# Optimization experiments

Hardware: AMD Instinct MI355X
Metric: run time of the kernel (lower is better)

Reference implementation:

```python
import jax, jax.numpy as jnp
import numpy as np

K = 128      # scratch_keys_dim
NP = 3       # n_pointers
P = 200      # program_dim
STEPS = 3    # max_program_steps


def _positional_encoding(max_len=50, d=K):
    pos = np.arange(max_len, dtype=np.float32)[:, None]
    div = np.exp(np.arange(0, d, 2, dtype=np.float32) * (-np.log(10000.0) / d))
    pe = np.zeros((max_len, d), dtype=np.float32)
    pe[:, 0::2] = np.sin(pos * div)
    pe[:, 1::2] = np.cos(pos * div)
    return jnp.asarray(pe)


def setup_inputs() -> dict:
    B, I, L, Vin, Vout = 256, 16, 50, 1000, 512
    H = K * NP
    key = jax.random.key(0)
    ks = jax.random.split(key, 8)
    s = 0.05
    return {
        'instructions': jax.random.randint(ks[0], (I, B), 0, Vin),
        'true_actions': jax.random.randint(ks[1], (L, B), 0, Vout),
        'gate_emb': jax.random.normal(ks[2], (Vin, 2), jnp.float32) * s,
        'program_emb': jax.random.normal(ks[3], (Vin, P), jnp.float32) * s,
        'primitive_emb': jax.random.normal(ks[4], (Vin, Vout), jnp.float32) * s,
        'w_ih': jax.random.normal(ks[5], (3 * H, P), jnp.float32) * s,
        'w_hh': jax.random.normal(ks[6], (3 * H, H), jnp.float32) * s,
        'b_ih': jnp.zeros((3 * H,), jnp.float32),
        'b_hh': jnp.zeros((3 * H,), jnp.float32),
        'scratch_keys': _positional_encoding(),
        'init_value': jnp.zeros((Vout,), jnp.float32).at[0].set(1.0),  # one-hot eos
    }


def _gru_cell(x, h, w_ih, w_hh, b_ih, b_hh):
    # torch.nn.GRUCell math
    gi = x @ w_ih.T + b_ih
    gh = h @ w_hh.T + b_hh
    i_r, i_z, i_n = jnp.split(gi, 3, axis=-1)
    h_r, h_z, h_n = jnp.split(gh, 3, axis=-1)
    r = jax.nn.sigmoid(i_r + h_r)
    z = jax.nn.sigmoid(i_z + h_z)
    n = jnp.tanh(i_n + r * h_n)
    return (1.0 - z) * n + z * h


def reference(instructions, true_actions, gate_emb, program_emb, primitive_emb,
              w_ih, w_hh, b_ih, b_hh, scratch_keys, init_value):
    I, B = instructions.shape
    L = true_actions.shape[0]
    keys = scratch_keys[:L]                                    # [L,K], broadcast over batch
    h0 = jnp.tile(scratch_keys[0], (B, NP))                    # [B,3K] init executor hidden
    v0 = jnp.broadcast_to(init_value, (B, L, init_value.shape[0]))  # [B,L,Vout]

    def outer(carry, word):
        h, vals = carry
        gate = jax.nn.softmax(gate_emb[word], axis=-1)         # [B,2] (softmax gate activation)
        program = program_emb[word]                            # [B,P]
        primitive = primitive_emb[word]                        # [B,Vout]
        for _ in range(STEPS):
            read_ptr = h[:, K:2 * K]                           # [B,K]
            write_ptr = h[:, 2 * K:3 * K]                      # [B,K]
            read_attn = jax.nn.softmax(jnp.einsum('bk,lk->bl', read_ptr, keys), axis=-1)
            read_value = jnp.einsum('bl,blv->bv', read_attn, vals)
            # gate-weighted mix of primitive and read value
            new_value = gate[:, :1] * primitive + gate[:, 1:] * read_value   # [B,Vout]
            write_mask = jax.nn.softmax(jnp.einsum('bk,lk->bl', write_ptr, keys), axis=-1)
            vals = write_mask[:, :, None] * new_value[:, None, :] + (1.0 - write_mask[:, :, None]) * vals
            h = _gru_cell(program, h, w_ih, w_hh, b_ih, b_hh)
        return (h, vals), None

    (h, vals), _ = jax.lax.scan(outer, (h0, v0), instructions)
    actions = jnp.transpose(jax.nn.log_softmax(vals, axis=-1), (0, 2, 1))  # [B,Vout,L]
    return actions, true_actions.T
```

## Files before the change

kernel.cpp:

```cpp
#include <hip/hip_runtime.h>
#include <math.h>

#define KK     128
#define HH     384
#define H3     1152
#define PP     200
#define LL     50
#define VV     512
#define BB     256
#define II     16
#define NSTEPS 3

#define NT     1024
#define GRUT   768
#define VP2    258
#define KQP    33

#define GH4G   12
#define GIG    13
#define WQ4H_UI (GH4G * 3 * 384 * 4)
#define WQI_UI  (GIG  * 3 * 384 * 4)

__device__ __forceinline__ int dot4(unsigned a, unsigned b, int c) {
    return __builtin_amdgcn_sdot4((int)a, (int)b, c, false);
}
__device__ __forceinline__ int dot8(unsigned a, unsigned b, int c) {
    return __builtin_amdgcn_sdot8((int)a, (int)b, c, false);
}
__device__ __forceinline__ float rcpf(float x) { return __builtin_amdgcn_rcpf(x); }
__device__ __forceinline__ float sigm(float x) { return rcpf(1.f + __expf(-x)); }
__device__ __forceinline__ float tanh_fast(float x) {
    float xc = fminf(fmaxf(x, -15.f), 15.f);
    float t = __expf(2.f * xc);
    return 1.f - 2.f * rcpf(t + 1.f);
}
__device__ __forceinline__ int q8(float x, float sc) {
    int q = (int)rintf(x * sc);
    return q < -127 ? -127 : (q > 127 ? 127 : q);
}
__device__ __forceinline__ int q4(float x, float sc) {
    int q = (int)rintf(x * sc);
    return q < -7 ? -7 : (q > 7 ? 7 : q);
}

__global__ void wmax_reduce(const float* __restrict__ w_hh,
                            const float* __restrict__ w_ih,
                            const float* __restrict__ prog_emb,
                            unsigned* __restrict__ scales)
{
    int idx = blockIdx.x * 256 + threadIdx.x;
    int stride = gridDim.x * 256;
    float mh = 0.f, mi = 0.f, mp = 0.f;
    for (int i = idx; i < HH * H3; i += stride) mh = fmaxf(mh, fabsf(w_hh[i]));
    for (int i = idx; i < PP * H3; i += stride) mi = fmaxf(mi, fabsf(w_ih[i]));
    for (int i = idx; i < 1000 * PP; i += stride) mp = fmaxf(mp, fabsf(prog_emb[i]));
    #pragma unroll
    for (int mm = 32; mm >= 1; mm >>= 1) {
        mh = fmaxf(mh, __shfl_xor(mh, mm, 64));
        mi = fmaxf(mi, __shfl_xor(mi, mm, 64));
        mp = fmaxf(mp, __shfl_xor(mp, mm, 64));
    }
    if ((threadIdx.x & 63) == 0) {
        atomicMax(scales,     __float_as_uint(mh));
        atomicMax(scales + 1, __float_as_uint(mi));
        atomicMax(scales + 2, __float_as_uint(mp));
    }
}

__global__ void pack_weights(const float* __restrict__ w_hh,
                             const float* __restrict__ w_ih,
                             const unsigned* __restrict__ scales,
                             unsigned* __restrict__ wq)
{
    int idx = blockIdx.x * 256 + threadIdx.x;
    if (idx < WQ4H_UI) {
        const float sc = 7.f * rcpf(fmaxf(__uint_as_float(scales[0]), 1e-20f));
        int u4 = idx >> 2, m = idx & 3;
        int g = u4 / (3 * 384);
        int r = u4 - g * (3 * 384);
        int s = r / 384, t = r - s * 384;
        int j = t + 384 * s, k = 32 * g + 8 * m;
        const float* wr = w_hh + (long)j * HH + k;
        unsigned pw = 0;
        #pragma unroll
        for (int e = 0; e < 8; ++e) pw |= ((unsigned)(q4(wr[e], sc) & 0xF)) << (4 * e);
        wq[idx] = pw;
    } else if (idx < WQ4H_UI + WQI_UI) {
        const float sc = 127.f * rcpf(fmaxf(__uint_as_float(scales[1]), 1e-20f));
        int q = idx - WQ4H_UI;
        int u4 = q >> 2, m = q & 3;
        int g = u4 / (3 * 384);
        int r = u4 - g * (3 * 384);
        int s = r / 384, t = r - s * 384;
        int j = t + 384 * s, k = 16 * g + 4 * m;
        unsigned pw = 0;
        #pragma unroll
        for (int e = 0; e < 4; ++e) {
            float w = (k + e < PP) ? w_ih[(long)j * PP + k + e] : 0.f;
            pw |= ((unsigned)(q8(w, sc) & 255)) << (8 * e);
        }
        wq[WQ4H_UI + u4 * 4 + m] = pw;
    }
}

struct __align__(16) Smem {
    float2 vals[LL * VP2];
    unsigned keysq[LL * KQP + 16] __attribute__((aligned(16)));
    unsigned hq4[2][48]     __attribute__((aligned(16)));
    unsigned hq8[2][96]     __attribute__((aligned(16)));
    unsigned progq[56]      __attribute__((aligned(16)));
    float  raw[4][52], wmw[4][52];
    float  rowoff[52];
    float  partial[4 * 52];
};

__global__ __launch_bounds__(NT)
void symop_main(const int* __restrict__ instr,
                const float* __restrict__ gate_emb,
                const float* __restrict__ program_emb,
                const float* __restrict__ primitive_emb,
                const uint4* __restrict__ wqhh,
                const uint4* __restrict__ wqih,
                const unsigned* __restrict__ scales,
                const float* __restrict__ b_ih,
                const float* __restrict__ b_hh,
                const float* __restrict__ keys_g,
                const float* __restrict__ init_value,
                float* __restrict__ out)
{
    __shared__ Smem sm;

    const int tid  = threadIdx.x;
    const int lane = tid & 63;
    const int wid  = tid >> 6;
    const int b    = blockIdx.x;
    const int gl   = tid >> 1;
    const int koff = tid & 1;

    const float maxH = fmaxf(__uint_as_float(scales[0]), 1e-20f);
    const float maxI = fmaxf(__uint_as_float(scales[1]), 1e-20f);
    const float maxP = fmaxf(__uint_as_float(scales[2]), 1e-20f);
    const float ghs = maxH * (1.f / 49.f);
    const float gis = maxI * maxP * (1.f / 16129.f);
    const float psc = 127.f * rcpf(maxP);
    const float lsc = 1.f / 16129.f;

    float hcur = 0.f;
    if (tid < GRUT) hcur = keys_g[gl & 127];
    for (int idx = tid; idx < LL * 32; idx += NT) {
        int l = idx >> 5, kk = idx & 31;
        const float* kr = keys_g + l * KK + 4 * kk;
        unsigned pw = 0;
        #pragma unroll
        for (int e = 0; e < 4; ++e) pw |= ((unsigned)(q8(kr[e], 127.f) & 255)) << (8 * e);
        sm.keysq[l * KQP + kk] = pw;
    }
    if (tid < 96) {
        unsigned pw = 0;
        #pragma unroll
        for (int e = 0; e < 4; ++e) {
            int q = q8(keys_g[(4 * tid + e) & 127], 127.f);
            pw |= ((unsigned)(q & 255)) << (8 * e);
        }
        sm.hq8[0][tid] = pw;
    } else if (tid >= 128 && tid < 128 + 48) {
        int u = tid - 128;
        unsigned pw = 0;
        #pragma unroll
        for (int e = 0; e < 8; ++e) {
            int q = q4(keys_g[(8 * u + e) & 127], 7.f);
            pw |= ((unsigned)(q & 0xF)) << (4 * e);
        }
        sm.hq4[0][u] = pw;
    }
    for (int idx = tid; idx < LL * 256; idx += NT) {
        int l = idx >> 8, c = idx & 255;
        sm.vals[l * VP2 + c] = *(const float2*)(init_value + 2 * c);
    }
    if (tid >= GRUT && tid < GRUT + 52) {
        int qt = tid - GRUT;
        int w0 = instr[b];
        const float* pg = program_emb + (long)w0 * PP;
        unsigned pw = 0;
        #pragma unroll
        for (int e = 0; e < 4; ++e) {
            int k = 4 * qt + e;
            float v = (k < PP) ? pg[k] : 0.f;
            pw |= ((unsigned)(q8(v, psc) & 255)) << (8 * e);
        }
        sm.progq[qt] = pw;
    }
    __syncthreads();

    float bh0 = 0, bh1 = 0, bh2 = 0, bi0 = 0, bi1 = 0, bi2 = 0;
    if (tid < GRUT) {
        bh0 = b_hh[gl]; bh1 = b_hh[gl + HH]; bh2 = b_hh[gl + 2 * HH];
        bi0 = b_ih[gl]; bi1 = b_ih[gl + HH]; bi2 = b_ih[gl + 2 * HH];
    }
    float gic0 = 0, gic1 = 0, gic2 = 0;
    int   gn0 = 0, gn1 = 0, gn2 = 0;

    if (tid < GRUT) {
        int ia0 = 0, ia1 = 0, ia2 = 0;
        const uint4* wi = wqih + gl;
        const int gs = koff ? 7 : 0, ge = koff ? GIG : 7;
        for (int g = gs; g < ge; ++g) {
            uint4 w0 = wi[(g * 3 + 0) * 384];
            uint4 w1 = wi[(g * 3 + 1) * 384];
            uint4 w2 = wi[(g * 3 + 2) * 384];
            uint4 hp = *(const uint4*)(sm.progq + 4 * g);
            ia0 = dot4(w0.x, hp.x, ia0); ia0 = dot4(w0.y, hp.y, ia0);
            ia0 = dot4(w0.z, hp.z, ia0); ia0 = dot4(w0.w, hp.w, ia0);
            ia1 = dot4(w1.x, hp.x, ia1); ia1 = dot4(w1.y, hp.y, ia1);
            ia1 = dot4(w1.z, hp.z, ia1); ia1 = dot4(w1.w, hp.w, ia1);
            ia2 = dot4(w2.x, hp.x, ia2); ia2 = dot4(w2.y, hp.y, ia2);
            ia2 = dot4(w2.z, hp.z, ia2); ia2 = dot4(w2.w, hp.w, ia2);
        }
        ia0 += __shfl_xor(ia0, 1, 64);
        ia1 += __shfl_xor(ia1, 1, 64);
        ia2 += __shfl_xor(ia2, 1, 64);
        gic0 = bi0 + (float)ia0 * gis;
        gic1 = bi1 + (float)ia1 * gis;
        gic2 = bi2 + (float)ia2 * gis;
    }

    int par = 0;
    for (int i = 0; i < II; ++i) {
        const int word = instr[i * BB + b];
        for (int t = 0; t < NSTEPS; ++t) {
            if (tid < GRUT) {
                int ia0 = 0, ia1 = 0, ia2 = 0;
                const uint4* wp = wqhh + gl;
                const int gb = koff * 6;
                #pragma unroll 2
                for (int gg = 0; gg < 6; ++gg) {
                    const int g = gb + gg;
                    uint4 w0 = wp[(g * 3 + 0) * 384];
                    uint4 w1 = wp[(g * 3 + 1) * 384];
                    uint4 w2 = wp[(g * 3 + 2) * 384];
                    uint4 hp = *(const uint4*)(sm.hq4[par] + 4 * g);
                    ia0 = dot8(w0.x, hp.x, ia0); ia0 = dot8(w0.y, hp.y, ia0);
                    ia0 = dot8(w0.z, hp.z, ia0); ia0 = dot8(w0.w, hp.w, ia0);
                    ia1 = dot8(w1.x, hp.x, ia1); ia1 = dot8(w1.y, hp.y, ia1);
                    ia1 = dot8(w1.z, hp.z, ia1); ia1 = dot8(w1.w, hp.w, ia1);
                    ia2 = dot8(w2.x, hp.x, ia2); ia2 = dot8(w2.y, hp.y, ia2);
                    ia2 = dot8(w2.z, hp.z, ia2); ia2 = dot8(w2.w, hp.w, ia2);
                }
                ia0 += __shfl_xor(ia0, 1, 64);
                ia1 += __shfl_xor(ia1, 1, 64);
                ia2 += __shfl_xor(ia2, 1, 64);
                const float gh0 = bh0 + (float)ia0 * ghs;
                const float gh1 = bh1 + (float)ia1 * ghs;
                const float gh2 = bh2 + (float)ia2 * ghs;

                if (i + 1 < II) {
                    const uint4* wi = wqih + gl;
                    if (t == 1) {
                        gn0 = 0; gn1 = 0; gn2 = 0;
                        if (!koff) {
                            #pragma unroll 2
                            for (int g = 0; g < 7; ++g) {
                                uint4 w0 = wi[(g * 3 + 0) * 384];
                                uint4 w1 = wi[(g * 3 + 1) * 384];
                                uint4 w2 = wi[(g * 3 + 2) * 384];
                                uint4 hp = *(const uint4*)(sm.progq + 4 * g);
                                gn0 = dot4(w0.x, hp.x, gn0); gn0 = dot4(w0.y, hp.y, gn0);
                                gn0 = dot4(w0.z, hp.z, gn0); gn0 = dot4(w0.w, hp.w, gn0);
                                gn1 = dot4(w1.x, hp.x, gn1); gn1 = dot4(w1.y, hp.y, gn1);
                                gn1 = dot4(w1.z, hp.z, gn1); gn1 = dot4(w1.w, hp.w, gn1);
                                gn2 = dot4(w2.x, hp.x, gn2); gn2 = dot4(w2.y, hp.y, gn2);
                                gn2 = dot4(w2.z, hp.z, gn2); gn2 = dot4(w2.w, hp.w, gn2);
                            }
                        }
                    } else if (t == 2) {
                        if (koff) {
                            #pragma unroll 2
                            for (int g = 7; g < GIG; ++g) {
                                uint4 w0 = wi[(g * 3 + 0) * 384];
                                uint4 w1 = wi[(g * 3 + 1) * 384];
                                uint4 w2 = wi[(g * 3 + 2) * 384];
                                uint4 hp = *(const uint4*)(sm.progq + 4 * g);
                                gn0 = dot4(w0.x, hp.x, gn0); gn0 = dot4(w0.y, hp.y, gn0);
                                gn0 = dot4(w0.z, hp.z, gn0); gn0 = dot4(w0.w, hp.w, gn0);
                                gn1 = dot4(w1.x, hp.x, gn1); gn1 = dot4(w1.y, hp.y, gn1);
                                gn1 = dot4(w1.z, hp.z, gn1); gn1 = dot4(w1.w, hp.w, gn1);
                                gn2 = dot4(w2.x, hp.x, gn2); gn2 = dot4(w2.y, hp.y, gn2);
                                gn2 = dot4(w2.z, hp.z, gn2); gn2 = dot4(w2.w, hp.w, gn2);
                            }
                        }
                        const int f0 = gn0 + __shfl_xor(gn0, 1, 64);
                        const int f1 = gn1 + __shfl_xor(gn1, 1, 64);
                        const int f2 = gn2 + __shfl_xor(gn2, 1, 64);
                        gic0 = bi0 + (float)f0 * gis;
                        gic1 = bi1 + (float)f1 * gis;
                        gic2 = bi2 + (float)f2 * gis;
                    }
                }

                const float r = sigm(gic0 + gh0);
                const float z = sigm(gic1 + gh1);
                const float n = tanh_fast(gic2 + r * gh2);
                const float hn = (1.f - z) * n + z * hcur;
                hcur = hn;
                int q8v = ((int)rintf(hn * 127.f)) & 255;
                unsigned v1 = (unsigned)q8v | ((unsigned)(__shfl_down(q8v, 2, 64) & 255) << 8);
                unsigned v2 = v1 | ((unsigned)__shfl_down((int)v1, 4, 64) << 16);
                if (!(tid & 7)) sm.hq8[par ^ 1][tid >> 3] = v2;
                int q4v = ((int)rintf(hn * 7.f)) & 0xF;
                unsigned u1 = (unsigned)q4v | ((unsigned)(__shfl_down(q4v, 2, 64) & 0xF) << 4);
                unsigned u2 = u1 | ((unsigned)(__shfl_down((int)u1, 4, 64) & 0xFF) << 8);
                unsigned u4 = u2 | ((unsigned)__shfl_down((int)u2, 8, 64) << 16);
                if (!(tid & 15)) sm.hq4[par ^ 1][tid >> 4] = u4;
            } else {
                const int w4 = wid - 12;
                float rlog = -1e30f, wlog = -1e30f;
                if (lane < LL) {
                    int ir = 0, iw = 0;
                    const unsigned* kq = sm.keysq + lane * KQP;
                    const uint4* h8r = (const uint4*)(sm.hq8[par] + 32);
                    const uint4* h8w = (const uint4*)(sm.hq8[par] + 64);
                    #pragma unroll
                    for (int o = 0; o < 8; ++o) {
                        uint4 hr = h8r[o], hw = h8w[o];
                        unsigned k0 = kq[4 * o], k1 = kq[4 * o + 1];
                        unsigned k2 = kq[4 * o + 2], k3 = kq[4 * o + 3];
                        ir = dot4(k0, hr.x, ir); ir = dot4(k1, hr.y, ir);
                        ir = dot4(k2, hr.z, ir); ir = dot4(k3, hr.w, ir);
                        iw = dot4(k0, hw.x, iw); iw = dot4(k1, hw.y, iw);
                        iw = dot4(k2, hw.z, iw); iw = dot4(k3, hw.w, iw);
                    }
                    rlog = (float)ir * lsc;
                    wlog = (float)iw * lsc;
                }
                float mr = rlog, mw = wlog;
                #pragma unroll
                for (int mm = 32; mm >= 1; mm >>= 1) {
                    mr = fmaxf(mr, __shfl_xor(mr, mm, 64));
                    mw = fmaxf(mw, __shfl_xor(mw, mm, 64));
                }
                float er = (lane < LL) ? __expf(rlog - mr) : 0.f;
                float ew = (lane < LL) ? __expf(wlog - mw) : 0.f;
                float sr = er, sw = ew;
                #pragma unroll
                for (int mm = 32; mm >= 1; mm >>= 1) {
                    sr += __shfl_xor(sr, mm, 64);
                    sw += __shfl_xor(sw, mm, 64);
                }
                if (lane < LL) {
                    sm.raw[w4][lane] = er * rcpf(sr);
                    sm.wmw[w4][lane] = ew * rcpf(sw);
                }
                const float ge0 = gate_emb[2 * word], ge1 = gate_emb[2 * word + 1];
                const float gmx = fmaxf(ge0, ge1);
                const float e0 = __expf(ge0 - gmx), e1 = __expf(ge1 - gmx);
                const float g0 = e0 * rcpf(e0 + e1), g1 = 1.0f - g0;
                const float* prim = primitive_emb + (long)word * VV;

                const int c = tid - GRUT;
                float2 pr = *(const float2*)(prim + 2 * c);
                float rv0 = 0.f, rv1 = 0.f;
                #pragma unroll 10
                for (int l = 0; l < LL; ++l) {
                    float2 vv = sm.vals[l * VP2 + c];
                    rv0 = fmaf(sm.raw[w4][l], vv.x, rv0);
                    rv1 = fmaf(sm.raw[w4][l], vv.y, rv1);
                }
                const float nv0 = g0 * pr.x + g1 * rv0;
                const float nv1 = g0 * pr.y + g1 * rv1;
                #pragma unroll 10
                for (int l = 0; l < LL; ++l) {
                    float2 vv = sm.vals[l * VP2 + c];
                    const float w = sm.wmw[w4][l];
                    vv.x = fmaf(w, nv0 - vv.x, vv.x);
                    vv.y = fmaf(w, nv1 - vv.y, vv.y);
                    sm.vals[l * VP2 + c] = vv;
                }
                if (t == 0 && i + 1 < II && tid < GRUT + 52) {
                    int qt = tid - GRUT;
                    int wn = instr[(i + 1) * BB + b];
                    const float* pg = program_emb + (long)wn * PP;
                    unsigned pw = 0;
                    #pragma unroll
                    for (int e = 0; e < 4; ++e) {
                        int k = 4 * qt + e;
                        float v = (k < PP) ? pg[k] : 0.f;
                        pw |= ((unsigned)(q8(v, psc) & 255)) << (8 * e);
                    }
                    sm.progq[qt] = pw;
                }
            }
            __syncthreads();
            par ^= 1;
        }
    }

    if (tid < 256) {
        #pragma unroll 5
        for (int l = 0; l < LL; ++l) {
            float2 vv = sm.vals[l * VP2 + tid];
            float e = __expf(vv.x) + __expf(vv.y);
            #pragma unroll
            for (int mm = 32; mm >= 1; mm >>= 1) e += __shfl_xor(e, mm, 64);
            if (lane == 0) sm.partial[wid * 52 + l] = e;
        }
    }
    __syncthreads();
    if (tid < LL) {
        float s = 0.f;
        #pragma unroll
        for (int w = 0; w < 4; ++w) s += sm.partial[w * 52 + tid];
        sm.rowoff[tid] = logf(s);
    }
    __syncthreads();

    if (tid < 256) {
        float* ob0 = out + (long)b * VV * LL + (long)(2 * tid) * LL;
        float* ob1 = ob0 + LL;
        #pragma unroll 5
        for (int l = 0; l < LL; l += 2) {
            float2 va = sm.vals[l * VP2 + tid];
            float2 vb = sm.vals[(l + 1) * VP2 + tid];
            float o0 = sm.rowoff[l], o1 = sm.rowoff[l + 1];
            *(float2*)(ob0 + l) = make_float2(va.x - o0, vb.x - o1);
            *(float2*)(ob1 + l) = make_float2(va.y - o0, vb.y - o1);
        }
    }
}

__global__ void ta_copy(const int* __restrict__ ta, float* __restrict__ out2)
{
    int idx = blockIdx.x * 256 + threadIdx.x;
    if (idx < BB * LL) {
        int b2 = idx / LL, l = idx % LL;
        out2[idx] = (float)ta[l * BB + b2];
    }
}

extern "C" void kernel_launch(void* const* d_in, const int* in_sizes, int n_in,
                              void* d_out, int out_size, void* d_ws, size_t ws_size,
                              hipStream_t stream)
{
    const int*   instr        = (const int*)  d_in[0];
    const int*   true_actions = (const int*)  d_in[1];
    const float* gate_emb     = (const float*)d_in[2];
    const float* program_emb  = (const float*)d_in[3];
    const float* primitive_emb= (const float*)d_in[4];
    const float* w_ih         = (const float*)d_in[5];
    const float* w_hh         = (const float*)d_in[6];
    const float* b_ih         = (const float*)d_in[7];
    const float* b_hh         = (const float*)d_in[8];
    const float* scratch_keys = (const float*)d_in[9];
    const float* init_value   = (const float*)d_in[10];

    unsigned* scales = (unsigned*)d_ws;
    unsigned* wq     = (unsigned*)d_ws + 4;
    const uint4* wqhh = (const uint4*)wq;
    const uint4* wqih = (const uint4*)(wq + WQ4H_UI);

    hipMemsetAsync(scales, 0, 12, stream);
    wmax_reduce<<<256, 256, 0, stream>>>(w_hh, w_ih, program_emb, scales);
    {
        int total = WQ4H_UI + WQI_UI;
        pack_weights<<<(total + 255) / 256, 256, 0, stream>>>(w_hh, w_ih, scales, wq);
    }

    float* out = (float*)d_out;
    float* out_actions = out;
    float* out_ta      = out + (long)BB * VV * LL;

    symop_main<<<BB, NT, 0, stream>>>(instr, gate_emb, program_emb, primitive_emb,
                                      wqhh, wqih, scales, b_ih, b_hh,
                                      scratch_keys, init_value, out_actions);

    ta_copy<<<(BB * LL + 255) / 256, 256, 0, stream>>>(true_actions, out_ta);
}
```

Baseline: 343.3 us.

## Interleave packed GRU weights per thread and compute next input gates in one step

Packed int4 hidden-weight and int8 input-weight tiles are re-laid out so each thread indexes weights by tid with stride 768. Adjacent lanes, which hold the two K-halves of the same row, now read contiguous uint4s, giving better-coalesced global loads. The next instruction's input-gate projection is now computed entirely at step 1 by both K-halves, not split across steps 1 and 2, and its result is held in separate registers until step 2. Both halves now do balanced work, at the cost of padding the input weights with zeros and adding an extra barrier after the prologue.

```diff
diff --git a/kernel.cpp b/kernel.cpp
--- a/kernel.cpp
+++ b/kernel.cpp
@@ -16,10 +16,9 @@
 #define VP2    258
 #define KQP    33
 
-#define GH4G   12
 #define GIG    13
-#define WQ4H_UI (GH4G * 3 * 384 * 4)
-#define WQI_UI  (GIG  * 3 * 384 * 4)
+#define WQ4H_UI (6 * 3 * 768 * 4)
+#define WQI_UI  (7 * 3 * 768 * 4)
 
 __device__ __forceinline__ int dot4(unsigned a, unsigned b, int c) {
     return __builtin_amdgcn_sdot4((int)a, (int)b, c, false);
@@ -76,10 +75,12 @@
     if (idx < WQ4H_UI) {
         const float sc = 7.f * rcpf(fmaxf(__uint_as_float(scales[0]), 1e-20f));
         int u4 = idx >> 2, m = idx & 3;
-        int g = u4 / (3 * 384);
-        int r = u4 - g * (3 * 384);
-        int s = r / 384, t = r - s * 384;
-        int j = t + 384 * s, k = 32 * g + 8 * m;
+        int gg = u4 / (3 * 768);
+        int r  = u4 - gg * (3 * 768);
+        int s  = r / 768, tt = r - s * 768;
+        int gl = tt >> 1, ko = tt & 1;
+        int j = gl + 384 * s;
+        int k = (ko * 6 + gg) * 32 + 8 * m;
         const float* wr = w_hh + (long)j * HH + k;
         unsigned pw = 0;
         #pragma unroll
@@ -89,15 +90,20 @@
         const float sc = 127.f * rcpf(fmaxf(__uint_as_float(scales[1]), 1e-20f));
         int q = idx - WQ4H_UI;
         int u4 = q >> 2, m = q & 3;
-        int g = u4 / (3 * 384);
-        int r = u4 - g * (3 * 384);
-        int s = r / 384, t = r - s * 384;
-        int j = t + 384 * s, k = 16 * g + 4 * m;
-        unsigned pw = 0;
-        #pragma unroll
-        for (int e = 0; e < 4; ++e) {
-            float w = (k + e < PP) ? w_ih[(long)j * PP + k + e] : 0.f;
-            pw |= ((unsigned)(q8(w, sc) & 255)) << (8 * e);
+        int gg = u4 / (3 * 768);
+        int r  = u4 - gg * (3 * 768);
+        int s  = r / 768, tt = r - s * 768;
+        int gl = tt >> 1, ko = tt & 1;
+        int g = ko ? 7 + gg : gg;
+        int j = gl + 384 * s;
+        unsigned pw = 0;
+        if (g < GIG) {
+            int k = 16 * g + 4 * m;
+            #pragma unroll
+            for (int e = 0; e < 4; ++e) {
+                float w = (k + e < PP) ? w_ih[(long)j * PP + k + e] : 0.f;
+                pw |= ((unsigned)(q8(w, sc) & 255)) << (8 * e);
+            }
         }
         wq[WQ4H_UI + u4 * 4 + m] = pw;
     }
@@ -198,17 +204,18 @@
         bi0 = b_ih[gl]; bi1 = b_ih[gl + HH]; bi2 = b_ih[gl + 2 * HH];
     }
     float gic0 = 0, gic1 = 0, gic2 = 0;
-    int   gn0 = 0, gn1 = 0, gn2 = 0;
+    float gnf0 = 0, gnf1 = 0, gnf2 = 0;
 
     if (tid < GRUT) {
         int ia0 = 0, ia1 = 0, ia2 = 0;
-        const uint4* wi = wqih + gl;
-        const int gs = koff ? 7 : 0, ge = koff ? GIG : 7;
-        for (int g = gs; g < ge; ++g) {
-            uint4 w0 = wi[(g * 3 + 0) * 384];
-            uint4 w1 = wi[(g * 3 + 1) * 384];
-            uint4 w2 = wi[(g * 3 + 2) * 384];
-            uint4 hp = *(const uint4*)(sm.progq + 4 * g);
+        const uint4* wi = wqih + tid;
+        #pragma unroll 2
+        for (int gg = 0; gg < 7; ++gg) {
+            uint4 w0 = wi[(gg * 3 + 0) * 768];
+            uint4 w1 = wi[(gg * 3 + 1) * 768];
+            uint4 w2 = wi[(gg * 3 + 2) * 768];
+            int g = koff ? 7 + gg : gg;
+            uint4 hp = *(const uint4*)(sm.progq + 4 * ((g < GIG) ? g : 0));
             ia0 = dot4(w0.x, hp.x, ia0); ia0 = dot4(w0.y, hp.y, ia0);
             ia0 = dot4(w0.z, hp.z, ia0); ia0 = dot4(w0.w, hp.w, ia0);
             ia1 = dot4(w1.x, hp.x, ia1); ia1 = dot4(w1.y, hp.y, ia1);
@@ -223,6 +230,7 @@
         gic1 = bi1 + (float)ia1 * gis;
         gic2 = bi2 + (float)ia2 * gis;
     }
+    __syncthreads();
 
     int par = 0;
     for (int i = 0; i < II; ++i) {
@@ -230,15 +238,13 @@
         for (int t = 0; t < NSTEPS; ++t) {
             if (tid < GRUT) {
                 int ia0 = 0, ia1 = 0, ia2 = 0;
-                const uint4* wp = wqhh + gl;
-                const int gb = koff * 6;
+                const uint4* wp = wqhh + tid;
                 #pragma unroll 2
                 for (int gg = 0; gg < 6; ++gg) {
-                    const int g = gb + gg;
-                    uint4 w0 = wp[(g * 3 + 0) * 384];
-                    uint4 w1 = wp[(g * 3 + 1) * 384];
-                    uint4 w2 = wp[(g * 3 + 2) * 384];
-                    uint4 hp = *(const uint4*)(sm.hq4[par] + 4 * g);
+                    uint4 w0 = wp[(gg * 3 + 0) * 768];
+                    uint4 w1 = wp[(gg * 3 + 1) * 768];
+                    uint4 w2 = wp[(gg * 3 + 2) * 768];
+                    uint4 hp = *(const uint4*)(sm.hq4[par] + 4 * (koff * 6 + gg));
                     ia0 = dot8(w0.x, hp.x, ia0); ia0 = dot8(w0.y, hp.y, ia0);
                     ia0 = dot8(w0.z, hp.z, ia0); ia0 = dot8(w0.w, hp.w, ia0);
                     ia1 = dot8(w1.x, hp.x, ia1); ia1 = dot8(w1.y, hp.y, ia1);
@@ -253,48 +259,29 @@
                 const float gh1 = bh1 + (float)ia1 * ghs;
                 const float gh2 = bh2 + (float)ia2 * ghs;
 
-                if (i + 1 < II) {
-                    const uint4* wi = wqih + gl;
-                    if (t == 1) {
-                        gn0 = 0; gn1 = 0; gn2 = 0;
-                        if (!koff) {
-                            #pragma unroll 2
-                            for (int g = 0; g < 7; ++g) {
-                                uint4 w0 = wi[(g * 3 + 0) * 384];
-                                uint4 w1 = wi[(g * 3 + 1) * 384];
-                                uint4 w2 = wi[(g * 3 + 2) * 384];
-                                uint4 hp = *(const uint4*)(sm.progq + 4 * g);
-                                gn0 = dot4(w0.x, hp.x, gn0); gn0 = dot4(w0.y, hp.y, gn0);
-                                gn0 = dot4(w0.z, hp.z, gn0); gn0 = dot4(w0.w, hp.w, gn0);
-                                gn1 = dot4(w1.x, hp.x, gn1); gn1 = dot4(w1.y, hp.y, gn1);
-                                gn1 = dot4(w1.z, hp.z, gn1); gn1 = dot4(w1.w, hp.w, gn1);
-                                gn2 = dot4(w2.x, hp.x, gn2); gn2 = dot4(w2.y, hp.y, gn2);
-                                gn2 = dot4(w2.z, hp.z, gn2); gn2 = dot4(w2.w, hp.w, gn2);
-                            }
-                        }
-                    } else if (t == 2) {
-                        if (koff) {
-                            #pragma unroll 2
-                            for (int g = 7; g < GIG; ++g) {
-                                uint4 w0 = wi[(g * 3 + 0) * 384];
-                                uint4 w1 = wi[(g * 3 + 1) * 384];
-                                uint4 w2 = wi[(g * 3 + 2) * 384];
-                                uint4 hp = *(const uint4*)(sm.progq + 4 * g);
-                                gn0 = dot4(w0.x, hp.x, gn0); gn0 = dot4(w0.y, hp.y, gn0);
-                                gn0 = dot4(w0.z, hp.z, gn0); gn0 = dot4(w0.w, hp.w, gn0);
-                                gn1 = dot4(w1.x, hp.x, gn1); gn1 = dot4(w1.y, hp.y, gn1);
-                                gn1 = dot4(w1.z, hp.z, gn1); gn1 = dot4(w1.w, hp.w, gn1);
-                                gn2 = dot4(w2.x, hp.x, gn2); gn2 = dot4(w2.y, hp.y, gn2);
-                                gn2 = dot4(w2.z, hp.z, gn2); gn2 = dot4(w2.w, hp.w, gn2);
-                            }
-                        }
-                        const int f0 = gn0 + __shfl_xor(gn0, 1, 64);
-                        const int f1 = gn1 + __shfl_xor(gn1, 1, 64);
-                        const int f2 = gn2 + __shfl_xor(gn2, 1, 64);
-                        gic0 = bi0 + (float)f0 * gis;
-                        gic1 = bi1 + (float)f1 * gis;
-                        gic2 = bi2 + (float)f2 * gis;
+                if (t == 1 && i + 1 < II) {
+                    int j0 = 0, j1 = 0, j2 = 0;
+                    const uint4* wi = wqih + tid;
+                    #pragma unroll 2
+                    for (int gg = 0; gg < 7; ++gg) {
+                        uint4 w0 = wi[(gg * 3 + 0) * 768];
+                        uint4 w1 = wi[(gg * 3 + 1) * 768];
+                        uint4 w2 = wi[(gg * 3 + 2) * 768];
+                        int g = koff ? 7 + gg : gg;
+                        uint4 hp = *(const uint4*)(sm.progq + 4 * ((g < GIG) ? g : 0));
+                        j0 = dot4(w0.x, hp.x, j0); j0 = dot4(w0.y, hp.y, j0);
+                        j0 = dot4(w0.z, hp.z, j0); j0 = dot4(w0.w, hp.w, j0);
+                        j1 = dot4(w1.x, hp.x, j1); j1 = dot4(w1.y, hp.y, j1);
+                        j1 = dot4(w1.z, hp.z, j1); j1 = dot4(w1.w, hp.w, j1);
+                        j2 = dot4(w2.x, hp.x, j2); j2 = dot4(w2.y, hp.y, j2);
+                        j2 = dot4(w2.z, hp.z, j2); j2 = dot4(w2.w, hp.w, j2);
                     }
+                    j0 += __shfl_xor(j0, 1, 64);
+                    j1 += __shfl_xor(j1, 1, 64);
+                    j2 += __shfl_xor(j2, 1, 64);
+                    gnf0 = bi0 + (float)j0 * gis;
+                    gnf1 = bi1 + (float)j1 * gis;
+                    gnf2 = bi2 + (float)j2 * gis;
                 }
 
                 const float r = sigm(gic0 + gh0);
@@ -311,6 +298,10 @@
                 unsigned u2 = u1 | ((unsigned)(__shfl_down((int)u1, 4, 64) & 0xFF) << 8);
                 unsigned u4 = u2 | ((unsigned)__shfl_down((int)u2, 8, 64) << 16);
                 if (!(tid & 15)) sm.hq4[par ^ 1][tid >> 4] = u4;
+
+                if (t == 2 && i + 1 < II) {
+                    gic0 = gnf0; gic1 = gnf1; gic2 = gnf2;
+                }
             } else {
                 const int w4 = wid - 12;
                 float rlog = -1e30f, wlog = -1e30f;
```

Result: faster. 305.6 us (-11.0%).
